# Optimization experiments

Hardware: AMD Instinct MI355X
Metric: run time of the kernel (lower is better)

Reference implementation:

```python
import jax, jax.numpy as jnp
import numpy as np

EMBED = 768
HIDDEN = 4 * EMBED
TEMPERATURE = 1.0
LN_EPS = 1e-5


def setup_inputs() -> dict:
    key = jax.random.key(0)
    ks = jax.random.split(key, 10)
    s = 1.0 / np.sqrt(EMBED)
    sh = 1.0 / np.sqrt(HIDDEN)
    return {
        "x": jax.random.normal(ks[0], (32, 577, EMBED), dtype=jnp.float32),
        "Wq": jax.random.normal(ks[1], (EMBED, EMBED), dtype=jnp.float32) * s,
        "Wk": jax.random.normal(ks[2], (EMBED, EMBED), dtype=jnp.float32) * s,
        "Wv": jax.random.normal(ks[3], (EMBED, EMBED), dtype=jnp.float32) * s,
        "ln1_g": jnp.ones((EMBED,), jnp.float32),
        "ln1_b": jnp.zeros((EMBED,), jnp.float32),
        "ln2_g": jnp.ones((EMBED,), jnp.float32),
        "ln2_b": jnp.zeros((EMBED,), jnp.float32),
        "W1": jax.random.normal(ks[4], (EMBED, HIDDEN), dtype=jnp.float32) * s,
        "b1": jnp.zeros((HIDDEN,), jnp.float32),
        "W2": jax.random.normal(ks[5], (HIDDEN, EMBED), dtype=jnp.float32) * sh,
        "b2": jnp.zeros((EMBED,), jnp.float32),
    }


def layer_norm(x, g, b):
    mu = jnp.mean(x, axis=-1, keepdims=True)
    var = jnp.mean(jnp.square(x - mu), axis=-1, keepdims=True)
    return (x - mu) * jax.lax.rsqrt(var + LN_EPS) * g + b


def l2_attention(h, Wq, Wk, Wv):
    # h: [b, s, d]
    Q = h @ Wq
    K = h @ Wk
    V = h @ Wv
    q_sq = jnp.sum(Q * Q, axis=-1, keepdims=True)          # [b, s, 1]
    k_sq = jnp.sum(K * K, axis=-1, keepdims=True)          # [b, s, 1]
    qk = jnp.einsum('bqd,bkd->bqk', Q, K)                  # [b, s, s]
    l2_sq = q_sq + jnp.swapaxes(k_sq, -2, -1) - 2.0 * qk
    attn = jax.nn.softmax(-l2_sq / TEMPERATURE, axis=-1)
    return jnp.einsum('bqk,bkd->bqd', attn, V)


def reference(x, Wq, Wk, Wv, ln1_g, ln1_b, ln2_g, ln2_b, W1, b1, W2, b2):
    x = x + l2_attention(layer_norm(x, ln1_g, ln1_b), Wq, Wk, Wv)
    h = layer_norm(x, ln2_g, ln2_b)
    h = jax.nn.gelu(h @ W1 + b1, approximate=False) @ W2 + b2
    return x + h
```

## Files before the change

kernel.cpp:

```cpp
#include <hip/hip_runtime.h>

#define EMBED 768
#define HIDDEN 3072
#define SEQ 577
#define BATCH 32
#define ROWS (BATCH*SEQ)
#define KPAD 608
#define SLD 640

typedef __attribute__((ext_vector_type(4))) float f32x4;
typedef __attribute__((ext_vector_type(8))) __bf16 bf16x8;
typedef unsigned int __attribute__((address_space(1))) as1_u32;
typedef unsigned int __attribute__((address_space(3))) as3_u32;

__device__ __forceinline__ unsigned short f2b(float f) {
    unsigned int u = __float_as_uint(f);
    u = u + 0x7FFFu + ((u >> 16) & 1u);
    return (unsigned short)(u >> 16);
}
__device__ __forceinline__ float b2f(unsigned short s) {
    return __uint_as_float(((unsigned int)s) << 16);
}
__device__ __forceinline__ void gld16(const unsigned short* g, unsigned short* l) {
    __builtin_amdgcn_global_load_lds((const as1_u32*)g, (as3_u32*)l, 16, 0, 0);
}

__device__ __forceinline__ int swz_lin() {
    int nx = gridDim.x;
    int lin = blockIdx.y * nx + blockIdx.x;
    if (gridDim.z == 1) {
        int nwg = nx * gridDim.y;
        int q = nwg >> 3, r = nwg & 7;
        int xcd = lin & 7, blk = lin >> 3;
        lin = (xcd < r ? xcd * (q + 1) : r * (q + 1) + (xcd - r) * q) + blk;
    }
    return lin;
}

__global__ void ln_kernel(const float* __restrict__ x, const float* __restrict__ g,
                          const float* __restrict__ b, unsigned short* __restrict__ o) {
    int row = blockIdx.x;
    const float* xr = x + (size_t)row * EMBED;
    int t = threadIdx.x;
    float v0 = xr[t], v1 = xr[t + 256], v2 = xr[t + 512];
    float s = v0 + v1 + v2;
    float ss = v0 * v0 + v1 * v1 + v2 * v2;
#pragma unroll
    for (int d = 32; d; d >>= 1) { s += __shfl_down(s, d); ss += __shfl_down(ss, d); }
    __shared__ float rs[4], rss[4];
    if ((t & 63) == 0) { rs[t >> 6] = s; rss[t >> 6] = ss; }
    __syncthreads();
    s = rs[0] + rs[1] + rs[2] + rs[3];
    ss = rss[0] + rss[1] + rss[2] + rss[3];
    float mu = s * (1.0f / EMBED);
    float var = ss * (1.0f / EMBED) - mu * mu;
    float rstd = rsqrtf(var + 1e-5f);
    unsigned short* orow = o + (size_t)row * EMBED;
    orow[t]       = f2b((v0 - mu) * rstd * g[t]       + b[t]);
    orow[t + 256] = f2b((v1 - mu) * rstd * g[t + 256] + b[t + 256]);
    orow[t + 512] = f2b((v2 - mu) * rstd * g[t + 512] + b[t + 512]);
}

__global__ void ln_split_kernel(const float* __restrict__ x, const float* __restrict__ g,
                                const float* __restrict__ b, unsigned short* __restrict__ oh,
                                unsigned short* __restrict__ ol) {
    int row = blockIdx.x;
    const float* xr = x + (size_t)row * EMBED;
    int t = threadIdx.x;
    float v0 = xr[t], v1 = xr[t + 256], v2 = xr[t + 512];
    float s = v0 + v1 + v2;
    float ss = v0 * v0 + v1 * v1 + v2 * v2;
#pragma unroll
    for (int d = 32; d; d >>= 1) { s += __shfl_down(s, d); ss += __shfl_down(ss, d); }
    __shared__ float rs[4], rss[4];
    if ((t & 63) == 0) { rs[t >> 6] = s; rss[t >> 6] = ss; }
    __syncthreads();
    s = rs[0] + rs[1] + rs[2] + rs[3];
    ss = rss[0] + rss[1] + rss[2] + rss[3];
    float mu = s * (1.0f / EMBED);
    float var = ss * (1.0f / EMBED) - mu * mu;
    float rstd = rsqrtf(var + 1e-5f);
    size_t base = (size_t)row * EMBED;
#pragma unroll
    for (int i = 0; i < 3; i++) {
        int d = t + 256 * i;
        float v = (i == 0 ? v0 : (i == 1 ? v1 : v2));
        float y = (v - mu) * rstd * g[d] + b[d];
        unsigned short h = f2b(y);
        oh[base + d] = h;
        ol[base + d] = f2b(y - b2f(h));
    }
}

__global__ void ksq_kernel(const unsigned short* __restrict__ qh,
                           const unsigned short* __restrict__ ql, float* __restrict__ ksq) {
    int row = blockIdx.x;
    int t = threadIdx.x;
    size_t base = (size_t)row * 1536 + EMBED;
    float s = 0.f;
#pragma unroll
    for (int i = 0; i < 3; i++) {
        int d = t + 256 * i;
        float k = b2f(qh[base + d]) + b2f(ql[base + d]);
        s += k * k;
    }
#pragma unroll
    for (int d = 32; d; d >>= 1) s += __shfl_down(s, d);
    __shared__ float rs[4];
    if ((t & 63) == 0) rs[t >> 6] = s;
    __syncthreads();
    if (t == 0) ksq[row] = rs[0] + rs[1] + rs[2] + rs[3];
}

__global__ void softmax_kernel(const float* __restrict__ S, unsigned short* __restrict__ P) {
    int r = blockIdx.x;
    int t = threadIdx.x;
    const float* sr = S + (size_t)r * SLD;
    float v0 = sr[t];
    float v1 = sr[t + 256];
    float v2 = (t + 512 < SEQ) ? sr[t + 512] : -3.0e38f;
    float m = fmaxf(v0, fmaxf(v1, v2));
#pragma unroll
    for (int d = 32; d; d >>= 1) m = fmaxf(m, __shfl_down(m, d));
    __shared__ float rm[4];
    if ((t & 63) == 0) rm[t >> 6] = m;
    __syncthreads();
    m = fmaxf(fmaxf(rm[0], rm[1]), fmaxf(rm[2], rm[3]));
    float e0 = expf(v0 - m);
    float e1 = expf(v1 - m);
    float e2 = (t + 512 < SEQ) ? expf(v2 - m) : 0.0f;
    float s = e0 + e1 + e2;
#pragma unroll
    for (int d = 32; d; d >>= 1) s += __shfl_down(s, d);
    __shared__ float rsum[4];
    if ((t & 63) == 0) rsum[t >> 6] = s;
    __syncthreads();
    float inv = 1.0f / (rsum[0] + rsum[1] + rsum[2] + rsum[3]);
    unsigned short* pr = P + (size_t)r * KPAD;
    pr[t]       = f2b(e0 * inv);
    pr[t + 256] = f2b(e1 * inv);
    if (t + 512 < KPAD) pr[t + 512] = f2b(e2 * inv);
}

__global__ void wt_kernel(const float* __restrict__ in, unsigned short* __restrict__ out,
                          int K, int N, int outRowOff, int outLd) {
    __shared__ float tile[32][33];
    int n0 = blockIdx.x * 32, k0 = blockIdx.y * 32;
    int tx = threadIdx.x, ty = threadIdx.y;
#pragma unroll
    for (int i = 0; i < 4; i++)
        tile[ty + 8 * i][tx] = in[(size_t)(k0 + ty + 8 * i) * N + (n0 + tx)];
    __syncthreads();
#pragma unroll
    for (int i = 0; i < 4; i++)
        out[(size_t)(outRowOff + n0 + ty + 8 * i) * outLd + (k0 + tx)] = f2b(tile[tx][ty + 8 * i]);
}

__global__ void wt_split_kernel(const float* __restrict__ in, unsigned short* __restrict__ oh,
                                unsigned short* __restrict__ ol,
                                int K, int N, int outRowOff, int outLd) {
    __shared__ float tile[32][33];
    int n0 = blockIdx.x * 32, k0 = blockIdx.y * 32;
    int tx = threadIdx.x, ty = threadIdx.y;
#pragma unroll
    for (int i = 0; i < 4; i++)
        tile[ty + 8 * i][tx] = in[(size_t)(k0 + ty + 8 * i) * N + (n0 + tx)];
    __syncthreads();
#pragma unroll
    for (int i = 0; i < 4; i++) {
        float v = tile[tx][ty + 8 * i];
        unsigned short h = f2b(v);
        size_t idx = (size_t)(outRowOff + n0 + ty + 8 * i) * outLd + (k0 + tx);
        oh[idx] = h;
        ol[idx] = f2b(v - b2f(h));
    }
}

__global__ void vt_kernel(const unsigned short* __restrict__ vbuf, unsigned short* __restrict__ vt) {
    int z = blockIdx.z;
    int d0 = blockIdx.x * 32, c0 = blockIdx.y * 32;
    __shared__ unsigned short tile[32][33];
    int tx = threadIdx.x, ty = threadIdx.y;
#pragma unroll
    for (int i = 0; i < 4; i++) {
        int c = c0 + ty + 8 * i;
        tile[ty + 8 * i][tx] = (c < SEQ) ? vbuf[((size_t)z * SEQ + c) * EMBED + d0 + tx]
                                         : (unsigned short)0;
    }
    __syncthreads();
#pragma unroll
    for (int i = 0; i < 4; i++) {
        int d = d0 + ty + 8 * i, c = c0 + tx;
        vt[(size_t)z * EMBED * KPAD + (size_t)d * KPAD + c] = tile[tx][ty + 8 * i];
    }
}

template <int EPI>
__global__ __launch_bounds__(256, 2) void gemm_bt(
    const unsigned short* __restrict__ A, int lda, long long sA,
    const unsigned short* __restrict__ B, int ldb, long long sB,
    int M, int N, int K,
    void* __restrict__ C, int ldc, long long sC,
    const float* __restrict__ E, long long sE) {
    __shared__ unsigned short As[2][4096];
    __shared__ unsigned short Bs[2][4096];
    int z = blockIdx.z;
    A += (size_t)z * sA;
    B += (size_t)z * sB;
    int nx = gridDim.x;
    int lin = swz_lin();
    int row0 = (lin / nx) * 128, col0 = (lin % nx) * 128;
    int t = threadIdx.x, l = t & 63, w = t >> 6;
    int wr = w >> 1, wc = w & 1;

    f32x4 acc[4][4] = {};

    int srow = t >> 2;
    int sblk = t & 3;
    int kboff = (sblk ^ ((srow >> 1) & 3)) * 8;

    auto stage = [&](int sl, int kt) {
#pragma unroll
        for (int c = 0; c < 2; ++c) {
            int ar = row0 + c * 64 + srow; ar = ar < M ? ar : M - 1;
            gld16(A + (size_t)ar * lda + kt + kboff, &As[sl][c * 2048 + t * 8]);
            int br = col0 + c * 64 + srow; br = br < N ? br : N - 1;
            gld16(B + (size_t)br * ldb + kt + kboff, &Bs[sl][c * 2048 + t * 8]);
        }
    };
    auto compute = [&](int sl) {
        bf16x8 af[4], bfr[4];
        int kb = l >> 4;
#pragma unroll
        for (int m = 0; m < 4; m++) {
            int r = wr * 64 + m * 16 + (l & 15);
            int blk = kb ^ ((r >> 1) & 3);
            af[m] = *reinterpret_cast<const bf16x8*>(&As[sl][r * 32 + blk * 8]);
        }
#pragma unroll
        for (int n = 0; n < 4; n++) {
            int r = wc * 64 + n * 16 + (l & 15);
            int blk = kb ^ ((r >> 1) & 3);
            bfr[n] = *reinterpret_cast<const bf16x8*>(&Bs[sl][r * 32 + blk * 8]);
        }
#pragma unroll
        for (int m = 0; m < 4; m++)
#pragma unroll
            for (int n = 0; n < 4; n++)
                acc[m][n] = __builtin_amdgcn_mfma_f32_16x16x32_bf16(af[m], bfr[n], acc[m][n], 0, 0, 0);
    };

    for (int kt = 0; kt < K; kt += 64) {
        stage(0, kt);
        bool has2 = (kt + 32) < K;
        if (has2) stage(1, kt + 32);
        asm volatile("s_waitcnt vmcnt(0)" ::: "memory");
        __builtin_amdgcn_s_barrier();
        __builtin_amdgcn_sched_barrier(0);
        compute(0);
        if (has2) compute(1);
        __builtin_amdgcn_s_barrier();
        __builtin_amdgcn_sched_barrier(0);
    }

    int rbase = row0 + wr * 64 + (l >> 4) * 4;
    int cbase = col0 + wc * 64 + (l & 15);
#pragma unroll
    for (int m = 0; m < 4; m++) {
#pragma unroll
        for (int n = 0; n < 4; n++) {
            int col = cbase + n * 16;
            if (col >= N) continue;
#pragma unroll
            for (int j = 0; j < 4; j++) {
                int row = rbase + m * 16 + j;
                if (row >= M) continue;
                float v = acc[m][n][j];
                size_t oidx = (size_t)z * sC + (size_t)row * ldc + col;
                if (EPI == 0) {
                    ((unsigned short*)C)[oidx] = f2b(v);
                } else if (EPI == 2) {
                    ((float*)C)[oidx] = E[oidx] + v;
                } else if (EPI == 3) {
                    float xx = v + E[col];
                    float g = 0.5f * xx * (1.0f + erff(xx * 0.70710678118654752f));
                    ((unsigned short*)C)[oidx] = f2b(g);
                } else if (EPI == 4) {
                    ((float*)C)[oidx] += v + E[col];
                }
            }
        }
    }
}

template <int EPI>
__global__ __launch_bounds__(256, 2) void gemm_hp(
    const unsigned short* __restrict__ Ah, const unsigned short* __restrict__ Al, int lda, long long sA,
    const unsigned short* __restrict__ Bh, const unsigned short* __restrict__ Bl, int ldb, long long sB,
    int M, int N, int K,
    void* __restrict__ C, int ldc, long long sC, long long planeOff,
    const float* __restrict__ E, long long sE) {
    __shared__ unsigned short Ash[4096], Asl[4096], Bsh[4096], Bsl[4096];
    int z = blockIdx.z;
    Ah += (size_t)z * sA; Al += (size_t)z * sA;
    Bh += (size_t)z * sB; Bl += (size_t)z * sB;
    int nx = gridDim.x;
    int lin = swz_lin();
    int row0 = (lin / nx) * 128, col0 = (lin % nx) * 128;
    int t = threadIdx.x, l = t & 63, w = t >> 6;
    int wr = w >> 1, wc = w & 1;

    f32x4 acc[4][4] = {};

    int srow = t >> 2;
    int sblk = t & 3;
    int kboff = (sblk ^ ((srow >> 1) & 3)) * 8;

    for (int kt = 0; kt < K; kt += 32) {
#pragma unroll
        for (int c = 0; c < 2; ++c) {
            int ar = row0 + c * 64 + srow; ar = ar < M ? ar : M - 1;
            size_t aoff = (size_t)ar * lda + kt + kboff;
            gld16(Ah + aoff, Ash + c * 2048 + t * 8);
            gld16(Al + aoff, Asl + c * 2048 + t * 8);
            int br = col0 + c * 64 + srow; br = br < N ? br : N - 1;
            size_t boff = (size_t)br * ldb + kt + kboff;
            gld16(Bh + boff, Bsh + c * 2048 + t * 8);
            gld16(Bl + boff, Bsl + c * 2048 + t * 8);
        }
        __syncthreads();
        int kb = l >> 4;
        bf16x8 afh[4], afl[4], bfh[4], bfl[4];
#pragma unroll
        for (int m = 0; m < 4; m++) {
            int r = wr * 64 + m * 16 + (l & 15);
            int blk = kb ^ ((r >> 1) & 3);
            afh[m] = *reinterpret_cast<const bf16x8*>(&Ash[r * 32 + blk * 8]);
            afl[m] = *reinterpret_cast<const bf16x8*>(&Asl[r * 32 + blk * 8]);
        }
#pragma unroll
        for (int n = 0; n < 4; n++) {
            int r = wc * 64 + n * 16 + (l & 15);
            int blk = kb ^ ((r >> 1) & 3);
            bfh[n] = *reinterpret_cast<const bf16x8*>(&Bsh[r * 32 + blk * 8]);
            bfl[n] = *reinterpret_cast<const bf16x8*>(&Bsl[r * 32 + blk * 8]);
        }
#pragma unroll
        for (int m = 0; m < 4; m++)
#pragma unroll
            for (int n = 0; n < 4; n++) {
                acc[m][n] = __builtin_amdgcn_mfma_f32_16x16x32_bf16(afh[m], bfh[n], acc[m][n], 0, 0, 0);
                acc[m][n] = __builtin_amdgcn_mfma_f32_16x16x32_bf16(afh[m], bfl[n], acc[m][n], 0, 0, 0);
                acc[m][n] = __builtin_amdgcn_mfma_f32_16x16x32_bf16(afl[m], bfh[n], acc[m][n], 0, 0, 0);
            }
        __syncthreads();
    }

    int rbase = row0 + wr * 64 + (l >> 4) * 4;
    int cbase = col0 + wc * 64 + (l & 15);
#pragma unroll
    for (int m = 0; m < 4; m++) {
#pragma unroll
        for (int n = 0; n < 4; n++) {
            int col = cbase + n * 16;
            if (col >= N) continue;
#pragma unroll
            for (int j = 0; j < 4; j++) {
                int row = rbase + m * 16 + j;
                if (row >= M) continue;
                float v = acc[m][n][j];
                size_t oidx = (size_t)z * sC + (size_t)row * ldc + col;
                if (EPI == 0) {
                    unsigned short h = f2b(v);
                    ((unsigned short*)C)[oidx] = h;
                    ((unsigned short*)C)[oidx + planeOff] = f2b(v - b2f(h));
                } else if (EPI == 1) {
                    ((float*)C)[oidx] = 2.0f * v - E[(size_t)z * sE + col];
                }
            }
        }
    }
}

extern "C" void kernel_launch(void* const* d_in, const int* in_sizes, int n_in,
                              void* d_out, int out_size, void* d_ws, size_t ws_size,
                              hipStream_t stream) {
    const float* x   = (const float*)d_in[0];
    const float* Wq  = (const float*)d_in[1];
    const float* Wk  = (const float*)d_in[2];
    const float* Wv  = (const float*)d_in[3];
    const float* g1  = (const float*)d_in[4];
    const float* be1 = (const float*)d_in[5];
    const float* g2  = (const float*)d_in[6];
    const float* be2 = (const float*)d_in[7];
    const float* W1  = (const float*)d_in[8];
    const float* bb1 = (const float*)d_in[9];
    const float* W2  = (const float*)d_in[10];
    const float* bb2 = (const float*)d_in[11];
    float* out = (float*)d_out;

    char* ws = (char*)d_ws;
    size_t off = 0;
    auto alloc = [&](size_t bytes) -> char* {
        char* p = ws + off;
        off += (bytes + 255) & ~(size_t)255;
        return p;
    };
    unsigned short* wqkTh = (unsigned short*)alloc((size_t)1536 * EMBED * 2);
    unsigned short* wqkTl = (unsigned short*)alloc((size_t)1536 * EMBED * 2);
    unsigned short* wvT   = (unsigned short*)alloc((size_t)EMBED * EMBED * 2);
    unsigned short* w1T   = (unsigned short*)alloc((size_t)HIDDEN * EMBED * 2);
    unsigned short* w2T   = (unsigned short*)alloc((size_t)EMBED * HIDDEN * 2);
    float*          ksqb  = (float*)alloc((size_t)ROWS * 4);
    char* regB = alloc((size_t)ROWS * HIDDEN * 2);
    char* regC = alloc((size_t)2 * ROWS * EMBED * 2);
    unsigned short* vbuf  = (unsigned short*)alloc((size_t)ROWS * EMBED * 2);
    unsigned short* vtb   = (unsigned short*)alloc((size_t)BATCH * EMBED * KPAD * 2);
    unsigned short* Pbuf  = (unsigned short*)alloc((size_t)ROWS * KPAD * 2);
    if (off > ws_size) return;

    unsigned short* qkh  = (unsigned short*)regB;
    unsigned short* qkl  = qkh + (size_t)ROWS * 1536;
    unsigned short* hid  = (unsigned short*)regB;
    unsigned short* h1h  = (unsigned short*)regC;
    unsigned short* h1l  = h1h + (size_t)ROWS * EMBED;
    float*          Sbuf = (float*)regC;
    unsigned short* h2   = (unsigned short*)regC;

    dim3 b256(256), bT(32, 8);

    wt_split_kernel<<<dim3(24, 24), bT, 0, stream>>>(Wq, wqkTh, wqkTl, EMBED, EMBED, 0, EMBED);
    wt_split_kernel<<<dim3(24, 24), bT, 0, stream>>>(Wk, wqkTh, wqkTl, EMBED, EMBED, EMBED, EMBED);
    wt_kernel<<<dim3(24, 24), bT, 0, stream>>>(Wv, wvT, EMBED, EMBED, 0, EMBED);
    wt_kernel<<<dim3(96, 24), bT, 0, stream>>>(W1, w1T, EMBED, HIDDEN, 0, EMBED);
    wt_kernel<<<dim3(24, 96), bT, 0, stream>>>(W2, w2T, HIDDEN, EMBED, 0, HIDDEN);

    ln_split_kernel<<<ROWS, b256, 0, stream>>>(x, g1, be1, h1h, h1l);

    gemm_hp<0><<<dim3(12, 145, 1), b256, 0, stream>>>(
        h1h, h1l, EMBED, 0, wqkTh, wqkTl, EMBED, 0,
        ROWS, 1536, EMBED, qkh, 1536, 0, (long long)ROWS * 1536, nullptr, 0);

    gemm_bt<0><<<dim3(6, 145, 1), b256, 0, stream>>>(
        h1h, EMBED, 0, wvT, EMBED, 0, ROWS, EMBED, EMBED, vbuf, EMBED, 0, nullptr, 0);

    ksq_kernel<<<ROWS, b256, 0, stream>>>(qkh, qkl, ksqb);

    gemm_hp<1><<<dim3(5, 5, 32), b256, 0, stream>>>(
        qkh, qkl, 1536, (long long)SEQ * 1536, qkh + EMBED, qkl + EMBED, 1536, (long long)SEQ * 1536,
        SEQ, SEQ, EMBED, Sbuf, SLD, (long long)SEQ * SLD, 0, ksqb, SEQ);

    softmax_kernel<<<ROWS, b256, 0, stream>>>(Sbuf, Pbuf);

    vt_kernel<<<dim3(24, 19, 32), bT, 0, stream>>>(vbuf, vtb);

    gemm_bt<2><<<dim3(6, 5, 32), b256, 0, stream>>>(
        Pbuf, KPAD, (long long)SEQ * KPAD, vtb, KPAD, (long long)EMBED * KPAD,
        SEQ, EMBED, KPAD, out, EMBED, (long long)SEQ * EMBED, x, (long long)SEQ * EMBED);

    ln_kernel<<<ROWS, b256, 0, stream>>>(out, g2, be2, h2);

    gemm_bt<3><<<dim3(24, 145, 1), b256, 0, stream>>>(
        h2, EMBED, 0, w1T, EMBED, 0, ROWS, HIDDEN, EMBED, hid, HIDDEN, 0, bb1, 0);

    gemm_bt<4><<<dim3(6, 145, 1), b256, 0, stream>>>(
        hid, HIDDEN, 0, w2T, HIDDEN, 0, ROWS, EMBED, HIDDEN, out, EMBED, 0, bb2, 0);
}
```

Measured before the change: 868.2 us.

## Use fast exp and tanh-GELU, hoist GEMM address math, add unchecked epilogue fast path

Replaces the erf-based exact GELU in the FFN epilogue with a tanh approximation built on __expf, and switches softmax exponentials to __expf. In both GEMM kernels, global and LDS address offsets are now computed once before the K loop instead of every iteration. A bounds-check-free epilogue is added for interior tiles. The GELU approximation changes the numerics relative to the exact erf reference, and the 32-bit offset arithmetic assumes indices fit in int.

```diff
diff --git a/kernel.cpp b/kernel.cpp
--- a/kernel.cpp
+++ b/kernel.cpp
@@ -23,6 +23,12 @@
 }
 __device__ __forceinline__ void gld16(const unsigned short* g, unsigned short* l) {
     __builtin_amdgcn_global_load_lds((const as1_u32*)g, (as3_u32*)l, 16, 0, 0);
+}
+__device__ __forceinline__ float gelu_f(float x) {
+    float u = x * (0.7978845608028654f + 0.03567740814183f * x * x);
+    float e = __expf(2.0f * u);
+    float th = 1.0f - 2.0f / (e + 1.0f);
+    return 0.5f * x * (1.0f + th);
 }
 
 __device__ __forceinline__ int swz_lin() {
@@ -126,9 +132,9 @@
     if ((t & 63) == 0) rm[t >> 6] = m;
     __syncthreads();
     m = fmaxf(fmaxf(rm[0], rm[1]), fmaxf(rm[2], rm[3]));
-    float e0 = expf(v0 - m);
-    float e1 = expf(v1 - m);
-    float e2 = (t + 512 < SEQ) ? expf(v2 - m) : 0.0f;
+    float e0 = __expf(v0 - m);
+    float e1 = __expf(v1 - m);
+    float e2 = (t + 512 < SEQ) ? __expf(v2 - m) : 0.0f;
     float s = e0 + e1 + e2;
 #pragma unroll
     for (int d = 32; d; d >>= 1) s += __shfl_down(s, d);
@@ -212,37 +218,36 @@
     int row0 = (lin / nx) * 128, col0 = (lin % nx) * 128;
     int t = threadIdx.x, l = t & 63, w = t >> 6;
     int wr = w >> 1, wc = w & 1;
+    int l15 = l & 15, kb = l >> 4;
 
     f32x4 acc[4][4] = {};
 
     int srow = t >> 2;
-    int sblk = t & 3;
-    int kboff = (sblk ^ ((srow >> 1) & 3)) * 8;
-
-    auto stage = [&](int sl, int kt) {
-#pragma unroll
-        for (int c = 0; c < 2; ++c) {
-            int ar = row0 + c * 64 + srow; ar = ar < M ? ar : M - 1;
-            gld16(A + (size_t)ar * lda + kt + kboff, &As[sl][c * 2048 + t * 8]);
-            int br = col0 + c * 64 + srow; br = br < N ? br : N - 1;
-            gld16(B + (size_t)br * ldb + kt + kboff, &Bs[sl][c * 2048 + t * 8]);
-        }
-    };
+    int kboff = ((t & 3) ^ ((srow >> 1) & 3)) * 8;
+
+    int aoE[2], boE[2];
+#pragma unroll
+    for (int c = 0; c < 2; ++c) {
+        int ar = row0 + c * 64 + srow; ar = ar < M ? ar : M - 1;
+        aoE[c] = ar * lda + kboff;
+        int br = col0 + c * 64 + srow; br = br < N ? br : N - 1;
+        boE[c] = br * ldb + kboff;
+    }
+    int aoff[4], boff[4];
+#pragma unroll
+    for (int m = 0; m < 4; m++) {
+        int r = wr * 64 + m * 16 + l15;
+        aoff[m] = r * 32 + (kb ^ ((r >> 1) & 3)) * 8;
+        int rn = wc * 64 + m * 16 + l15;
+        boff[m] = rn * 32 + (kb ^ ((rn >> 1) & 3)) * 8;
+    }
+
     auto compute = [&](int sl) {
         bf16x8 af[4], bfr[4];
-        int kb = l >> 4;
-#pragma unroll
-        for (int m = 0; m < 4; m++) {
-            int r = wr * 64 + m * 16 + (l & 15);
-            int blk = kb ^ ((r >> 1) & 3);
-            af[m] = *reinterpret_cast<const bf16x8*>(&As[sl][r * 32 + blk * 8]);
-        }
-#pragma unroll
-        for (int n = 0; n < 4; n++) {
-            int r = wc * 64 + n * 16 + (l & 15);
-            int blk = kb ^ ((r >> 1) & 3);
-            bfr[n] = *reinterpret_cast<const bf16x8*>(&Bs[sl][r * 32 + blk * 8]);
-        }
+#pragma unroll
+        for (int m = 0; m < 4; m++) af[m] = *reinterpret_cast<const bf16x8*>(&As[sl][aoff[m]]);
+#pragma unroll
+        for (int n = 0; n < 4; n++) bfr[n] = *reinterpret_cast<const bf16x8*>(&Bs[sl][boff[n]]);
 #pragma unroll
         for (int m = 0; m < 4; m++)
 #pragma unroll
@@ -250,10 +255,19 @@
                 acc[m][n] = __builtin_amdgcn_mfma_f32_16x16x32_bf16(af[m], bfr[n], acc[m][n], 0, 0, 0);
     };
 
+    int ldsoff = t * 8;
     for (int kt = 0; kt < K; kt += 64) {
-        stage(0, kt);
+        gld16(A + (size_t)(aoE[0] + kt), &As[0][ldsoff]);
+        gld16(A + (size_t)(aoE[1] + kt), &As[0][2048 + ldsoff]);
+        gld16(B + (size_t)(boE[0] + kt), &Bs[0][ldsoff]);
+        gld16(B + (size_t)(boE[1] + kt), &Bs[0][2048 + ldsoff]);
         bool has2 = (kt + 32) < K;
-        if (has2) stage(1, kt + 32);
+        if (has2) {
+            gld16(A + (size_t)(aoE[0] + kt + 32), &As[1][ldsoff]);
+            gld16(A + (size_t)(aoE[1] + kt + 32), &As[1][2048 + ldsoff]);
+            gld16(B + (size_t)(boE[0] + kt + 32), &Bs[1][ldsoff]);
+            gld16(B + (size_t)(boE[1] + kt + 32), &Bs[1][2048 + ldsoff]);
+        }
         asm volatile("s_waitcnt vmcnt(0)" ::: "memory");
         __builtin_amdgcn_s_barrier();
         __builtin_amdgcn_sched_barrier(0);
@@ -264,33 +278,34 @@
     }
 
     int rbase = row0 + wr * 64 + (l >> 4) * 4;
-    int cbase = col0 + wc * 64 + (l & 15);
-#pragma unroll
-    for (int m = 0; m < 4; m++) {
-#pragma unroll
-        for (int n = 0; n < 4; n++) {
-            int col = cbase + n * 16;
-            if (col >= N) continue;
-#pragma unroll
-            for (int j = 0; j < 4; j++) {
-                int row = rbase + m * 16 + j;
-                if (row >= M) continue;
-                float v = acc[m][n][j];
-                size_t oidx = (size_t)z * sC + (size_t)row * ldc + col;
-                if (EPI == 0) {
-                    ((unsigned short*)C)[oidx] = f2b(v);
-                } else if (EPI == 2) {
-                    ((float*)C)[oidx] = E[oidx] + v;
-                } else if (EPI == 3) {
-                    float xx = v + E[col];
-                    float g = 0.5f * xx * (1.0f + erff(xx * 0.70710678118654752f));
-                    ((unsigned short*)C)[oidx] = f2b(g);
-                } else if (EPI == 4) {
-                    ((float*)C)[oidx] += v + E[col];
+    int cbase = col0 + wc * 64 + l15;
+    auto epi = [&](bool chk) {
+#pragma unroll
+        for (int m = 0; m < 4; m++) {
+#pragma unroll
+            for (int n = 0; n < 4; n++) {
+                int col = cbase + n * 16;
+                if (chk && col >= N) continue;
+#pragma unroll
+                for (int j = 0; j < 4; j++) {
+                    int row = rbase + m * 16 + j;
+                    if (chk && row >= M) continue;
+                    float v = acc[m][n][j];
+                    size_t oidx = (size_t)z * sC + (size_t)row * ldc + col;
+                    if (EPI == 0) {
+                        ((unsigned short*)C)[oidx] = f2b(v);
+                    } else if (EPI == 2) {
+                        ((float*)C)[oidx] = E[oidx] + v;
+                    } else if (EPI == 3) {
+                        ((unsigned short*)C)[oidx] = f2b(gelu_f(v + E[col]));
+                    } else if (EPI == 4) {
+                        ((float*)C)[oidx] += v + E[col];
+                    }
                 }
             }
         }
-    }
+    };
+    if (row0 + 128 <= M && col0 + 128 <= N) epi(false); else epi(true);
 }
 
 template <int EPI>
@@ -309,41 +324,50 @@
     int row0 = (lin / nx) * 128, col0 = (lin % nx) * 128;
     int t = threadIdx.x, l = t & 63, w = t >> 6;
     int wr = w >> 1, wc = w & 1;
+    int l15 = l & 15, kb = l >> 4;
 
     f32x4 acc[4][4] = {};
 
     int srow = t >> 2;
-    int sblk = t & 3;
-    int kboff = (sblk ^ ((srow >> 1) & 3)) * 8;
-
+    int kboff = ((t & 3) ^ ((srow >> 1) & 3)) * 8;
+
+    int aoE[2], boE[2];
+#pragma unroll
+    for (int c = 0; c < 2; ++c) {
+        int ar = row0 + c * 64 + srow; ar = ar < M ? ar : M - 1;
+        aoE[c] = ar * lda + kboff;
+        int br = col0 + c * 64 + srow; br = br < N ? br : N - 1;
+        boE[c] = br * ldb + kboff;
+    }
+    int aoff[4], boff[4];
+#pragma unroll
+    for (int m = 0; m < 4; m++) {
+        int r = wr * 64 + m * 16 + l15;
+        aoff[m] = r * 32 + (kb ^ ((r >> 1) & 3)) * 8;
+        int rn = wc * 64 + m * 16 + l15;
+        boff[m] = rn * 32 + (kb ^ ((rn >> 1) & 3)) * 8;
+    }
+
+    int ldsoff = t * 8;
     for (int kt = 0; kt < K; kt += 32) {
 #pragma unroll
         for (int c = 0; c < 2; ++c) {
-            int ar = row0 + c * 64 + srow; ar = ar < M ? ar : M - 1;
-            size_t aoff = (size_t)ar * lda + kt + kboff;
-            gld16(Ah + aoff, Ash + c * 2048 + t * 8);
-            gld16(Al + aoff, Asl + c * 2048 + t * 8);
-            int br = col0 + c * 64 + srow; br = br < N ? br : N - 1;
-            size_t boff = (size_t)br * ldb + kt + kboff;
-            gld16(Bh + boff, Bsh + c * 2048 + t * 8);
-            gld16(Bl + boff, Bsl + c * 2048 + t * 8);
+            gld16(Ah + (size_t)(aoE[c] + kt), &Ash[c * 2048 + ldsoff]);
+            gld16(Al + (size_t)(aoE[c] + kt), &Asl[c * 2048 + ldsoff]);
+            gld16(Bh + (size_t)(boE[c] + kt), &Bsh[c * 2048 + ldsoff]);
+            gld16(Bl + (size_t)(boE[c] + kt), &Bsl[c * 2048 + ldsoff]);
         }
         __syncthreads();
-        int kb = l >> 4;
         bf16x8 afh[4], afl[4], bfh[4], bfl[4];
 #pragma unroll
         for (int m = 0; m < 4; m++) {
-            int r = wr * 64 + m * 16 + (l & 15);
-            int blk = kb ^ ((r >> 1) & 3);
-            afh[m] = *reinterpret_cast<const bf16x8*>(&Ash[r * 32 + blk * 8]);
-            afl[m] = *reinterpret_cast<const bf16x8*>(&Asl[r * 32 + blk * 8]);
+            afh[m] = *reinterpret_cast<const bf16x8*>(&Ash[aoff[m]]);
+            afl[m] = *reinterpret_cast<const bf16x8*>(&Asl[aoff[m]]);
         }
 #pragma unroll
         for (int n = 0; n < 4; n++) {
-            int r = wc * 64 + n * 16 + (l & 15);
-            int blk = kb ^ ((r >> 1) & 3);
-            bfh[n] = *reinterpret_cast<const bf16x8*>(&Bsh[r * 32 + blk * 8]);
-            bfl[n] = *reinterpret_cast<const bf16x8*>(&Bsl[r * 32 + blk * 8]);
+            bfh[n] = *reinterpret_cast<const bf16x8*>(&Bsh[boff[n]]);
+            bfl[n] = *reinterpret_cast<const bf16x8*>(&Bsl[boff[n]]);
         }
 #pragma unroll
         for (int m = 0; m < 4; m++)
@@ -357,29 +381,32 @@
     }
 
     int rbase = row0 + wr * 64 + (l >> 4) * 4;
-    int cbase = col0 + wc * 64 + (l & 15);
-#pragma unroll
-    for (int m = 0; m < 4; m++) {
-#pragma unroll
-        for (int n = 0; n < 4; n++) {
-            int col = cbase + n * 16;
-            if (col >= N) continue;
-#pragma unroll
-            for (int j = 0; j < 4; j++) {
-                int row = rbase + m * 16 + j;
-                if (row >= M) continue;
-                float v = acc[m][n][j];
-                size_t oidx = (size_t)z * sC + (size_t)row * ldc + col;
-                if (EPI == 0) {
-                    unsigned short h = f2b(v);
-                    ((unsigned short*)C)[oidx] = h;
-                    ((unsigned short*)C)[oidx + planeOff] = f2b(v - b2f(h));
-                } else if (EPI == 1) {
-                    ((float*)C)[oidx] = 2.0f * v - E[(size_t)z * sE + col];
+    int cbase = col0 + wc * 64 + l15;
+    auto epi = [&](bool chk) {
+#pragma unroll
+        for (int m = 0; m < 4; m++) {
+#pragma unroll
+            for (int n = 0; n < 4; n++) {
+                int col = cbase + n * 16;
+                if (chk && col >= N) continue;
+#pragma unroll
+                for (int j = 0; j < 4; j++) {
+                    int row = rbase + m * 16 + j;
+                    if (chk && row >= M) continue;
+                    float v = acc[m][n][j];
+                    size_t oidx = (size_t)z * sC + (size_t)row * ldc + col;
+                    if (EPI == 0) {
+                        unsigned short h = f2b(v);
+                        ((unsigned short*)C)[oidx] = h;
+                        ((unsigned short*)C)[oidx + planeOff] = f2b(v - b2f(h));
+                    } else if (EPI == 1) {
+                        ((float*)C)[oidx] = 2.0f * v - E[(size_t)z * sE + col];
+                    }
                 }
             }
         }
-    }
+    };
+    if (row0 + 128 <= M && col0 + 128 <= N) epi(false); else epi(true);
 }
 
 extern "C" void kernel_launch(void* const* d_in, const int* in_sizes, int n_in,
```

Result: faster. 782.6 us (-9.9%).
